# Performance work log

Measured on AMD Instinct MI355X. Metric: run time of the kernel, lower is better.

Reference implementation:

```python
import jax, jax.numpy as jnp
import numpy as np

B, T, N, E = 32, 512, 4, 16          # batch, seq_len, num_nodes, num_edges (N*N)
NI, EI = 16, 8                        # node / edge input channels
HN, HE, MH, C = 128, 128, 256, 8      # hidden node/edge, mlp hidden, classes

# complete-graph edge list (matches the src/dst double loop in __init__)
SRC = np.repeat(np.arange(N), N)      # [E]
DST = np.tile(np.arange(N), N)        # [E]
# GCNConv (PyG default) adds self-loops on top of the existing complete graph
# -> adjacency counts: off-diag 1, diag 2; in-degree of every node = N+1.
# symmetric norm deg^-1/2 A deg^-1/2 collapses to A/(N+1). Dense 4x4 matmul
# per graph is the efficient faithful form of the scatter-add here.
NORM_ADJ = (np.ones((N, N), np.float32) + np.eye(N, dtype=np.float32)) / (N + 1)


def lstm(x, Wih, Whh, b):
    """batch_first LSTM, torch gate order (i,f,g,o). x: [Bn,T,D] -> [Bn,T,H]."""
    H = Whh.shape[0]
    xz = x @ Wih + b  # precompute input projection [Bn,T,4H]

    def step(carry, zt):
        h, c = carry
        z = zt + h @ Whh
        i, f, g, o = jnp.split(z, 4, axis=-1)
        c = jax.nn.sigmoid(f) * c + jax.nn.sigmoid(i) * jnp.tanh(g)
        h = jax.nn.sigmoid(o) * jnp.tanh(c)
        return (h, c), h

    init = (jnp.zeros((x.shape[0], H), x.dtype), jnp.zeros((x.shape[0], H), x.dtype))
    _, hs = jax.lax.scan(step, init, jnp.swapaxes(xz, 0, 1))
    return jnp.swapaxes(hs, 0, 1)


def setup_inputs() -> dict:
    key = jax.random.key(0)
    ks = jax.random.split(key, 30)

    def p(k, shape, s=0.05):
        return (jax.random.normal(k, shape, jnp.float32) * s)

    return {
        "x_seq": jax.random.normal(ks[0], (B, T, N, NI), jnp.float32),
        "edge_attr_seq": jax.random.normal(ks[1], (B, T, E, EI), jnp.float32),
        "Wn1": p(ks[2], (NI, HN)), "bn1": p(ks[3], (HN,)),
        "Wn2": p(ks[4], (HN, HN)), "bn2": p(ks[5], (HN,)),
        "We1": p(ks[6], (EI, HE)), "be1": p(ks[7], (HE,)),
        "We2": p(ks[8], (HE, HE)), "be2": p(ks[9], (HE,)),
        "Wg1": p(ks[10], (HN, HN)), "bg1": p(ks[11], (HN,)),
        "Wg2": p(ks[12], (HN, HN)), "bg2": p(ks[13], (HN,)),
        "Wef1": p(ks[14], (HE, HE)), "bef1": p(ks[15], (HE,)),
        "Wef2": p(ks[16], (HE, HE)), "bef2": p(ks[17], (HE,)),
        "Wih_n": p(ks[18], (HN, 4 * HN)), "Whh_n": p(ks[19], (HN, 4 * HN)), "b_n": p(ks[20], (4 * HN,)),
        "Wih_e": p(ks[21], (HE, 4 * HE)), "Whh_e": p(ks[22], (HE, 4 * HE)), "b_e": p(ks[23], (4 * HE,)),
        "Wc1": p(ks[24], (2 * HN + HE, MH)), "bc1": p(ks[25], (MH,)),
        "Wc2": p(ks[26], (MH, C)), "bc2": p(ks[27], (C,)),
    }


def reference(x_seq, edge_attr_seq, Wn1, bn1, Wn2, bn2, We1, be1, We2, be2,
              Wg1, bg1, Wg2, bg2, Wef1, bef1, Wef2, bef2,
              Wih_n, Whh_n, b_n, Wih_e, Whh_e, b_e, Wc1, bc1, Wc2, bc2):
    adj = jnp.asarray(NORM_ADJ)
    # node / edge MLP embeddings
    x = jax.nn.relu(jax.nn.relu(x_seq @ Wn1 + bn1) @ Wn2 + bn2)      # [B,T,N,HN]
    e = jax.nn.relu(jax.nn.relu(edge_attr_seq @ We1 + be1) @ We2 + be2)  # [B,T,E,HE]
    # two GCN layers: normalized-adjacency aggregation per (batch,time) graph
    x = jax.nn.relu(jnp.einsum('ij,btjd->btid', adj, x @ Wg1) + bg1)
    x = jax.nn.relu(jnp.einsum('ij,btjd->btid', adj, x @ Wg2) + bg2)
    # edge FC stack
    e = jax.nn.relu(jax.nn.relu(e @ Wef1 + bef1) @ Wef2 + bef2)
    # LSTMs over time, one sequence per (batch, node) / (batch, edge)
    xn = x.transpose(0, 2, 1, 3).reshape(B * N, T, HN)
    en = e.transpose(0, 2, 1, 3).reshape(B * E, T, HE)
    hn = lstm(xn, Wih_n, Whh_n, b_n).reshape(B, N, T, HN).transpose(0, 2, 1, 3)  # [B,T,N,HN]
    he = lstm(en, Wih_e, Whh_e, b_e).reshape(B, E, T, HE).transpose(0, 2, 1, 3)  # [B,T,E,HE]
    # edge-gather classifier
    src_f = hn[:, :, jnp.asarray(SRC), :]
    dst_f = hn[:, :, jnp.asarray(DST), :]
    feats = jnp.concatenate([src_f, dst_f, he], axis=-1)  # [B,T,E,2HN+HE]
    logits = jax.nn.relu(feats @ Wc1 + bc1) @ Wc2 + bc2   # [B,T,E,C]
    return logits
```

## Files before the change

kernel.cpp:

```cpp
#include <hip/hip_runtime.h>
#include <cstdint>

constexpr int T_  = 512;
constexpr int HN_ = 128;

#define DEVI __device__ __forceinline__

typedef __bf16 bf16x8 __attribute__((ext_vector_type(8)));
typedef __bf16 bf16x4 __attribute__((ext_vector_type(4)));
typedef float  f32x4  __attribute__((ext_vector_type(4)));

DEVI float sigf(float x) { return __builtin_amdgcn_rcpf(1.f + __expf(-x)); }
DEVI float tanh_fast(float x) {
  return 1.f - 2.f * __builtin_amdgcn_rcpf(1.f + __expf(2.f * x));
}

DEVI void layer128_bf(const __bf16* __restrict__ src, __bf16* __restrict__ dst,
                      bf16x8 w0, bf16x8 w1, bf16x8 w2, bf16x8 w3,
                      float bv, int lm, int lh, int n)
{
  #pragma unroll
  for (int m = 0; m < 4; ++m) {
    const __bf16* sp = &src[(m*16 + lm)*136 + lh*8];
    const bf16x8 a0 = *reinterpret_cast<const bf16x8*>(sp);
    const bf16x8 a1 = *reinterpret_cast<const bf16x8*>(sp + 32);
    const bf16x8 a2 = *reinterpret_cast<const bf16x8*>(sp + 64);
    const bf16x8 a3 = *reinterpret_cast<const bf16x8*>(sp + 96);
    f32x4 acc = { bv, bv, bv, bv };
    acc = __builtin_amdgcn_mfma_f32_16x16x32_bf16(a0, w0, acc, 0, 0, 0);
    acc = __builtin_amdgcn_mfma_f32_16x16x32_bf16(a1, w1, acc, 0, 0, 0);
    acc = __builtin_amdgcn_mfma_f32_16x16x32_bf16(a2, w2, acc, 0, 0, 0);
    acc = __builtin_amdgcn_mfma_f32_16x16x32_bf16(a3, w3, acc, 0, 0, 0);
    #pragma unroll
    for (int r = 0; r < 4; ++r)
      dst[(m*16 + lh*4 + r)*136 + n] = (__bf16)fmaxf(acc[r], 0.f);
  }
}

DEVI void layer128_f32(const __bf16* __restrict__ src, float* __restrict__ dst,
                       bf16x8 w0, bf16x8 w1, bf16x8 w2, bf16x8 w3,
                       float bv, bool relu, int lm, int lh, int n)
{
  #pragma unroll
  for (int m = 0; m < 4; ++m) {
    const __bf16* sp = &src[(m*16 + lm)*136 + lh*8];
    const bf16x8 a0 = *reinterpret_cast<const bf16x8*>(sp);
    const bf16x8 a1 = *reinterpret_cast<const bf16x8*>(sp + 32);
    const bf16x8 a2 = *reinterpret_cast<const bf16x8*>(sp + 64);
    const bf16x8 a3 = *reinterpret_cast<const bf16x8*>(sp + 96);
    f32x4 acc = { bv, bv, bv, bv };
    acc = __builtin_amdgcn_mfma_f32_16x16x32_bf16(a0, w0, acc, 0, 0, 0);
    acc = __builtin_amdgcn_mfma_f32_16x16x32_bf16(a1, w1, acc, 0, 0, 0);
    acc = __builtin_amdgcn_mfma_f32_16x16x32_bf16(a2, w2, acc, 0, 0, 0);
    acc = __builtin_amdgcn_mfma_f32_16x16x32_bf16(a3, w3, acc, 0, 0, 0);
    #pragma unroll
    for (int r = 0; r < 4; ++r)
      dst[(m*16 + lh*4 + r)*132 + n] = relu ? fmaxf(acc[r], 0.f) : acc[r];
  }
}

__global__ __launch_bounds__(512, 4) void node_mlp_mfma_kernel(
    const float* __restrict__ x_seq,
    const float* __restrict__ Wn1, const float* __restrict__ bn1,
    const float* __restrict__ Wn2, const float* __restrict__ bn2,
    const float* __restrict__ Wg1, const float* __restrict__ bg1,
    const float* __restrict__ Wg2, const float* __restrict__ bg2,
    __bf16* __restrict__ xn)
{
  constexpr int P1 = 40;
  __shared__ __align__(16) __bf16 A1[64 * P1];
  __shared__ __align__(16) __bf16 Ab[64 * 136];
  __shared__ __align__(16) __bf16 Bb[64 * 136];
  __shared__ __align__(16) float  Yf[64 * 132];

  const int tid = threadIdx.x;
  const int w = tid >> 6, l = tid & 63, lm = l & 15, lh = l >> 4;
  const int n = w*16 + lm;

  bf16x8 w1, w2[4], w3[4], w4[4];
  const float b1 = bn1[n], b2 = bn2[n];
  #pragma unroll
  for (int j = 0; j < 8; ++j) {
    const int k = lh*8 + j;
    w1[j] = (k < 16) ? (__bf16)Wn1[k*128 + n] : (__bf16)0.f;
  }
  #pragma unroll
  for (int kt = 0; kt < 4; ++kt)
    #pragma unroll
    for (int j = 0; j < 8; ++j) {
      const int k = kt*32 + lh*8 + j;
      w2[kt][j] = (__bf16)Wn2[k*128 + n];
      w3[kt][j] = (__bf16)Wg1[k*128 + n];
      w4[kt][j] = (__bf16)Wg2[k*128 + n];
    }

  for (int i = tid; i < 64 * P1; i += 512) A1[i] = (__bf16)0.f;

  for (int g = blockIdx.x; g < 1024; g += 512) {
    #pragma unroll
    for (int it = 0; it < 2; ++it) {
      const int i = tid + it*512;
      A1[(i >> 4)*P1 + (i & 15)] = (__bf16)x_seq[(size_t)g*1024 + i];
    }
    __syncthreads();
    #pragma unroll
    for (int m = 0; m < 4; ++m) {
      const bf16x8 a = *reinterpret_cast<const bf16x8*>(&A1[(m*16+lm)*P1 + lh*8]);
      f32x4 acc = { b1, b1, b1, b1 };
      acc = __builtin_amdgcn_mfma_f32_16x16x32_bf16(a, w1, acc, 0, 0, 0);
      #pragma unroll
      for (int r = 0; r < 4; ++r)
        Ab[(m*16 + lh*4 + r)*136 + n] = (__bf16)fmaxf(acc[r], 0.f);
    }
    __syncthreads();
    layer128_bf(Ab, Bb, w2[0], w2[1], w2[2], w2[3], b2, lm, lh, n);
    __syncthreads();
    layer128_f32(Bb, Yf, w3[0], w3[1], w3[2], w3[3], 0.f, false, lm, lh, n);
    __syncthreads();
    #pragma unroll
    for (int it = 0; it < 4; ++it) {
      const int idx = tid + it*512;
      const int q = idx >> 7, d = idx & 127;
      const float y0 = Yf[(q*4+0)*132 + d], y1 = Yf[(q*4+1)*132 + d];
      const float y2 = Yf[(q*4+2)*132 + d], y3 = Yf[(q*4+3)*132 + d];
      const float s = y0 + y1 + y2 + y3;
      const float bv = bg1[d];
      Ab[(q*4+0)*136 + d] = (__bf16)fmaxf((s + y0)*0.2f + bv, 0.f);
      Ab[(q*4+1)*136 + d] = (__bf16)fmaxf((s + y1)*0.2f + bv, 0.f);
      Ab[(q*4+2)*136 + d] = (__bf16)fmaxf((s + y2)*0.2f + bv, 0.f);
      Ab[(q*4+3)*136 + d] = (__bf16)fmaxf((s + y3)*0.2f + bv, 0.f);
    }
    __syncthreads();
    layer128_f32(Ab, Yf, w4[0], w4[1], w4[2], w4[3], 0.f, false, lm, lh, n);
    __syncthreads();
    #pragma unroll
    for (int it = 0; it < 4; ++it) {
      const int idx = tid + it*512;
      const int q = idx >> 7, d = idx & 127;
      const int bt = g*16 + q, bb = bt >> 9, tt = bt & 511;
      const float y0 = Yf[(q*4+0)*132 + d], y1 = Yf[(q*4+1)*132 + d];
      const float y2 = Yf[(q*4+2)*132 + d], y3 = Yf[(q*4+3)*132 + d];
      const float s = y0 + y1 + y2 + y3;
      const float bv = bg2[d];
      xn[((size_t)(bb*4+0)*T_ + tt)*HN_ + d] = (__bf16)fmaxf((s + y0)*0.2f + bv, 0.f);
      xn[((size_t)(bb*4+1)*T_ + tt)*HN_ + d] = (__bf16)fmaxf((s + y1)*0.2f + bv, 0.f);
      xn[((size_t)(bb*4+2)*T_ + tt)*HN_ + d] = (__bf16)fmaxf((s + y2)*0.2f + bv, 0.f);
      xn[((size_t)(bb*4+3)*T_ + tt)*HN_ + d] = (__bf16)fmaxf((s + y3)*0.2f + bv, 0.f);
    }
    __syncthreads();
  }
}

__global__ __launch_bounds__(512, 4) void edge_mlp_mfma_kernel(
    const float* __restrict__ ea,
    const float* __restrict__ We1, const float* __restrict__ be1,
    const float* __restrict__ We2, const float* __restrict__ be2,
    const float* __restrict__ Wef1, const float* __restrict__ bef1,
    const float* __restrict__ Wef2, const float* __restrict__ bef2,
    __bf16* __restrict__ en)
{
  constexpr int P1 = 40;
  __shared__ __align__(16) __bf16 A1[64 * P1];
  __shared__ __align__(16) __bf16 Ab[64 * 136];
  __shared__ __align__(16) __bf16 Bb[64 * 136];
  __shared__ __align__(16) float  Of[64 * 132];

  const int tid = threadIdx.x;
  const int w = tid >> 6, l = tid & 63, lm = l & 15, lh = l >> 4;
  const int n = w*16 + lm;

  bf16x8 w1, w2[4], w3[4], w4[4];
  const float b1 = be1[n], b2 = be2[n], b3 = bef1[n], b4 = bef2[n];
  #pragma unroll
  for (int j = 0; j < 8; ++j) {
    const int k = lh*8 + j;
    w1[j] = (k < 8) ? (__bf16)We1[k*128 + n] : (__bf16)0.f;
  }
  #pragma unroll
  for (int kt = 0; kt < 4; ++kt)
    #pragma unroll
    for (int j = 0; j < 8; ++j) {
      const int k = kt*32 + lh*8 + j;
      w2[kt][j] = (__bf16)We2[k*128 + n];
      w3[kt][j] = (__bf16)Wef1[k*128 + n];
      w4[kt][j] = (__bf16)Wef2[k*128 + n];
    }

  for (int i = tid; i < 64 * P1; i += 512) A1[i] = (__bf16)0.f;

  for (int g = blockIdx.x; g < 4096; g += 512) {
    A1[(tid >> 3)*P1 + (tid & 7)] = (__bf16)ea[(size_t)g*512 + tid];
    __syncthreads();
    #pragma unroll
    for (int m = 0; m < 4; ++m) {
      const bf16x8 a = *reinterpret_cast<const bf16x8*>(&A1[(m*16+lm)*P1 + lh*8]);
      f32x4 acc = { b1, b1, b1, b1 };
      acc = __builtin_amdgcn_mfma_f32_16x16x32_bf16(a, w1, acc, 0, 0, 0);
      #pragma unroll
      for (int r = 0; r < 4; ++r)
        Ab[(m*16 + lh*4 + r)*136 + n] = (__bf16)fmaxf(acc[r], 0.f);
    }
    __syncthreads();
    layer128_bf(Ab, Bb, w2[0], w2[1], w2[2], w2[3], b2, lm, lh, n);
    __syncthreads();
    layer128_bf(Bb, Ab, w3[0], w3[1], w3[2], w3[3], b3, lm, lh, n);
    __syncthreads();
    layer128_f32(Ab, Of, w4[0], w4[1], w4[2], w4[3], b4, true, lm, lh, n);
    __syncthreads();
    #pragma unroll
    for (int i = 0; i < 4; ++i) {
      const int fi = tid + i*512;
      const int row = fi >> 5, c4 = fi & 31;
      const int q = row >> 4, e = row & 15;
      const int bt = g*4 + q, bb = bt >> 9, tt = bt & 511;
      const float4 v = *reinterpret_cast<const float4*>(&Of[row*132 + c4*4]);
      bf16x4 pk;
      pk[0]=(__bf16)v.x; pk[1]=(__bf16)v.y; pk[2]=(__bf16)v.z; pk[3]=(__bf16)v.w;
      *reinterpret_cast<bf16x4*>(
          &en[((size_t)(bb*16+e)*T_ + tt)*HN_ + c4*4]) = pk;
    }
    __syncthreads();
  }
}

__global__ __launch_bounds__(512, 2) void lstm_mfma_kernel(
    const float* __restrict__ Wih_n, const float* __restrict__ Whh_n,
    const float* __restrict__ b_n,
    const float* __restrict__ Wih_e, const float* __restrict__ Whh_e,
    const float* __restrict__ b_e,
    __bf16* __restrict__ xn, __bf16* __restrict__ en)
{
  __shared__ __align__(16) __bf16 ring[16 * 16 * 128];

  const bool is_node = (int)blockIdx.x < 8;
  const int  bidx    = is_node ? blockIdx.x : ((int)blockIdx.x - 8);
  const float* __restrict__ Wih  = is_node ? Wih_n : Wih_e;
  const float* __restrict__ Whh  = is_node ? Whh_n : Whh_e;
  const float* __restrict__ bias = is_node ? b_n   : b_e;
  __bf16* __restrict__ xh = (is_node ? xn : en) + (size_t)bidx * 16 * (T_ * HN_);

  const int tid = threadIdx.x;
  const int w   = tid >> 6;
  const int l   = tid & 63;
  const int lm  = l & 15;
  const int lh  = l >> 4;

  bf16x8 wih_f[4][4], whh_f[4][4];
  f32x4  bias_v[4];
  #pragma unroll
  for (int nt = 0; nt < 4; ++nt) {
    const int d   = w*16 + nt*4 + lh;
    bias_v[nt][0] = bias[0*128 + d];
    bias_v[nt][1] = bias[1*128 + d];
    bias_v[nt][2] = bias[2*128 + d];
    bias_v[nt][3] = bias[3*128 + d];
    const int col = (lm & 3)*128 + w*16 + nt*4 + (lm >> 2);
    #pragma unroll
    for (int kt = 0; kt < 4; ++kt)
      #pragma unroll
      for (int j = 0; j < 8; ++j) {
        const int k = kt*32 + lh*8 + j;
        wih_f[nt][kt][j] = (__bf16)Wih[k*512 + col];
        whh_f[nt][kt][j] = (__bf16)Whh[k*512 + col];
      }
  }

  {
    bf16x4 z; z[0]=z[1]=z[2]=z[3]=(__bf16)0.f;
    *reinterpret_cast<bf16x4*>(&ring[15*2048 + tid*4]) = z;
  }
  __syncthreads();

  const size_t seqStride = (size_t)T_ * HN_;
  const __bf16* __restrict__ xseq = xh + (size_t)lm * seqStride;

  f32x4 accsX[4];
  {
    bf16x8 bx[4];
    #pragma unroll
    for (int kt = 0; kt < 4; ++kt)
      bx[kt] = *reinterpret_cast<const bf16x8*>(&xseq[kt*32 + lh*8]);
    #pragma unroll
    for (int nt = 0; nt < 4; ++nt) {
      accsX[nt] = bias_v[nt];
      #pragma unroll
      for (int kt = 0; kt < 4; ++kt)
        accsX[nt] = __builtin_amdgcn_mfma_f32_16x16x32_bf16(wih_f[nt][kt], bx[kt], accsX[nt], 0, 0, 0);
    }
  }
  bf16x8 bxO[4], bxE[4];
  #pragma unroll
  for (int kt = 0; kt < 4; ++kt)
    bxO[kt] = *reinterpret_cast<const bf16x8*>(&xseq[(size_t)1*HN_ + kt*32 + lh*8]);

  float c[4] = {0.f, 0.f, 0.f, 0.f};

  #pragma unroll 2
  for (int t = 0; t < T_; ++t) {
    bf16x8* bxLoad = (t & 1) ? bxO : bxE;
    bf16x8* bxUse  = (t & 1) ? bxE : bxO;
    {
      const int tp = (t + 2 < T_) ? t + 2 : T_ - 1;
      #pragma unroll
      for (int kt = 0; kt < 4; ++kt)
        bxLoad[kt] = *reinterpret_cast<const bf16x8*>(
            &xseq[(size_t)tp*HN_ + kt*32 + lh*8]);
    }

    const int rbase = ((t + 15) & 15)*2048 + lm*128;
    bf16x8 bh[4];
    #pragma unroll
    for (int kt = 0; kt < 4; ++kt)
      bh[kt] = *reinterpret_cast<const bf16x8*>(
          &ring[rbase + (((kt*4 + lh) ^ (lm & 7)) << 3)]);

    #pragma unroll
    for (int nt = 0; nt < 4; ++nt)
      #pragma unroll
      for (int kt = 0; kt < 4; ++kt)
        accsX[nt] = __builtin_amdgcn_mfma_f32_16x16x32_bf16(whh_f[nt][kt], bh[kt], accsX[nt], 0, 0, 0);

    const int wbase = (t & 15)*2048 + lm*128;
    #pragma unroll
    for (int nt = 0; nt < 4; ++nt) {
      const float zi = accsX[nt][0], zf = accsX[nt][1];
      const float zg = accsX[nt][2], zo = accsX[nt][3];
      c[nt] = sigf(zf)*c[nt] + sigf(zi)*tanh_fast(zg);
      const float h = sigf(zo)*tanh_fast(c[nt]);
      const int up = (2*w + (nt >> 1)) ^ (lm & 7);
      ring[wbase + up*8 + (nt & 1)*4 + lh] = (__bf16)h;
    }

    #pragma unroll
    for (int nt = 0; nt < 4; ++nt) {
      accsX[nt] = bias_v[nt];
      #pragma unroll
      for (int kt = 0; kt < 4; ++kt)
        accsX[nt] = __builtin_amdgcn_mfma_f32_16x16x32_bf16(wih_f[nt][kt], bxUse[kt], accsX[nt], 0, 0, 0);
    }
    __syncthreads();

    if ((t & 15) == 15) {
      const int tb = t - 15;
      #pragma unroll
      for (int i = 0; i < 8; ++i) {
        const int uf = tid + i*512;
        const int tl = uf >> 8, sq = (uf >> 4) & 15, us = uf & 15;
        const int ulog = us ^ (sq & 7);
        const bf16x8 v = *reinterpret_cast<const bf16x8*>(
            &ring[tl*2048 + sq*128 + us*8]);
        *reinterpret_cast<bf16x8*>(
            &xh[(size_t)sq*seqStride + (size_t)(tb + tl)*HN_ + ulog*8]) = v;
      }
      __syncthreads();
    }
  }
}

__global__ __launch_bounds__(512, 1) void classifier_mfma_kernel(
    const __bf16* __restrict__ hn, const __bf16* __restrict__ he,
    const float* __restrict__ Wc1, const float* __restrict__ bc1,
    const float* __restrict__ Wc2, const float* __restrict__ bc2,
    float* __restrict__ out)
{
  constexpr int HP = 136;
  constexpr int DP = 264;
  __shared__ __align__(16) __bf16 hn_l[32 * HP];
  __shared__ __align__(16) __bf16 he_l[128 * HP];
  __shared__ __align__(16) __bf16 hid_l[128 * DP];

  const int tid = threadIdx.x;
  const int w   = tid >> 6;
  const int l   = tid & 63;
  const int lm  = l & 15;
  const int lh  = l >> 4;

  bf16x8 wb[2][12];
  float  bcol[2];
  #pragma unroll
  for (int jt = 0; jt < 2; ++jt) {
    const int j = w*32 + jt*16 + lm;
    bcol[jt] = bc1[j];
    #pragma unroll
    for (int kt = 0; kt < 12; ++kt)
      #pragma unroll
      for (int i = 0; i < 8; ++i)
        wb[jt][kt][i] = (__bf16)Wc1[(kt*32 + lh*8 + i)*256 + j];
  }
  bf16x8 wc2f[8];
  const float bc2v = (lm < 8) ? bc2[lm] : 0.f;
  #pragma unroll
  for (int kt = 0; kt < 8; ++kt)
    #pragma unroll
    for (int i = 0; i < 8; ++i)
      wc2f[kt][i] = (lm < 8) ? (__bf16)Wc2[(kt*32 + lh*8 + i)*8 + lm] : (__bf16)0.f;

  for (int g = blockIdx.x; g < 2048; g += 256) {
    const int b  = g >> 6;
    const int t0 = (g & 63) * 8;

    for (int u = tid; u < 2048; u += 512) {
      const int e = u >> 7, rem = u & 127;
      const int tt = rem >> 4, k = (rem & 15)*8;
      const bf16x8 v = *reinterpret_cast<const bf16x8*>(
          &he[((size_t)(b*16+e)*T_ + t0 + tt)*HN_ + k]);
      *reinterpret_cast<bf16x8*>(&he_l[(tt*16 + e)*HP + k]) = v;
    }
    for (int u = tid; u < 512; u += 512) {
      const int n = u >> 7, rem = u & 127;
      const int tt = rem >> 4, k = (rem & 15)*8;
      const bf16x8 v = *reinterpret_cast<const bf16x8*>(
          &hn[((size_t)(b*4+n)*T_ + t0 + tt)*HN_ + k]);
      *reinterpret_cast<bf16x8*>(&hn_l[(tt*4 + n)*HP + k]) = v;
    }
    __syncthreads();

    for (int tt = 0; tt < 8; ++tt) {
      bf16x8 af[12];
      #pragma unroll
      for (int kt = 0; kt < 4; ++kt)
        af[kt] = *reinterpret_cast<const bf16x8*>(
            &hn_l[(tt*4 + (lm>>2))*HP + kt*32 + lh*8]);
      #pragma unroll
      for (int kt = 0; kt < 4; ++kt)
        af[4+kt] = *reinterpret_cast<const bf16x8*>(
            &hn_l[(tt*4 + (lm&3))*HP + kt*32 + lh*8]);
      #pragma unroll
      for (int kt = 0; kt < 4; ++kt)
        af[8+kt] = *reinterpret_cast<const bf16x8*>(
            &he_l[(tt*16 + lm)*HP + kt*32 + lh*8]);
      #pragma unroll
      for (int jt = 0; jt < 2; ++jt) {
        f32x4 acc = { bcol[jt], bcol[jt], bcol[jt], bcol[jt] };
        #pragma unroll
        for (int kt = 0; kt < 12; ++kt)
          acc = __builtin_amdgcn_mfma_f32_16x16x32_bf16(af[kt], wb[jt][kt], acc, 0, 0, 0);
        #pragma unroll
        for (int r = 0; r < 4; ++r)
          hid_l[(tt*16 + lh*4 + r)*DP + (w*2 + jt)*16 + lm] = (__bf16)fmaxf(acc[r], 0.f);
      }
    }
    __syncthreads();

    {
      const int tt = w;
      f32x4 acc = { bc2v, bc2v, bc2v, bc2v };
      #pragma unroll
      for (int kt = 0; kt < 8; ++kt) {
        const bf16x8 a = *reinterpret_cast<const bf16x8*>(
            &hid_l[(tt*16 + lm)*DP + kt*32 + lh*8]);
        acc = __builtin_amdgcn_mfma_f32_16x16x32_bf16(a, wc2f[kt], acc, 0, 0, 0);
      }
      if (lm < 8) {
        const size_t bt = (size_t)b*T_ + t0 + tt;
        #pragma unroll
        for (int r = 0; r < 4; ++r)
          out[(bt*16 + lh*4 + r)*8 + lm] = acc[r];
      }
    }
    __syncthreads();
  }
}

extern "C" void kernel_launch(void* const* d_in, const int* in_sizes, int n_in,
                              void* d_out, int out_size, void* d_ws, size_t ws_size,
                              hipStream_t stream) {
  (void)in_sizes; (void)n_in; (void)out_size; (void)ws_size;
  const float* x_seq = (const float*)d_in[0];
  const float* ea    = (const float*)d_in[1];
  const float* Wn1 = (const float*)d_in[2];
  const float* bn1 = (const float*)d_in[3];
  const float* Wn2 = (const float*)d_in[4];
  const float* bn2 = (const float*)d_in[5];
  const float* We1 = (const float*)d_in[6];
  const float* be1 = (const float*)d_in[7];
  const float* We2 = (const float*)d_in[8];
  const float* be2 = (const float*)d_in[9];
  const float* Wg1 = (const float*)d_in[10];
  const float* bg1 = (const float*)d_in[11];
  const float* Wg2 = (const float*)d_in[12];
  const float* bg2 = (const float*)d_in[13];
  const float* Wef1 = (const float*)d_in[14];
  const float* bef1 = (const float*)d_in[15];
  const float* Wef2 = (const float*)d_in[16];
  const float* bef2 = (const float*)d_in[17];
  const float* Wih_n = (const float*)d_in[18];
  const float* Whh_n = (const float*)d_in[19];
  const float* b_n   = (const float*)d_in[20];
  const float* Wih_e = (const float*)d_in[21];
  const float* Whh_e = (const float*)d_in[22];
  const float* b_e   = (const float*)d_in[23];
  const float* Wc1 = (const float*)d_in[24];
  const float* bc1 = (const float*)d_in[25];
  const float* Wc2 = (const float*)d_in[26];
  const float* bc2 = (const float*)d_in[27];

  __bf16* xn = (__bf16*)d_ws;
  __bf16* en = xn + (size_t)128 * T_ * HN_;
  float* out = (float*)d_out;

  node_mlp_mfma_kernel<<<512, 512, 0, stream>>>(x_seq, Wn1, bn1, Wn2, bn2,
                                                Wg1, bg1, Wg2, bg2, xn);
  edge_mlp_mfma_kernel<<<512, 512, 0, stream>>>(ea, We1, be1, We2, be2,
                                                Wef1, bef1, Wef2, bef2, en);
  lstm_mfma_kernel<<<40, 512, 0, stream>>>(Wih_n, Whh_n, b_n,
                                           Wih_e, Whh_e, b_e, xn, en);
  classifier_mfma_kernel<<<256, 512, 0, stream>>>(xn, en, Wc1, bc1, Wc2, bc2, out);
}
```

Measured before the change: 779.5 us.

## Stage LSTM input chunks into LDS via async global_load_lds per 16 steps

The LSTM kernel now loads each 16-timestep chunk of input activations for all 16 sequences into a new LDS buffer with global_load_lds, instead of each lane issuing per-step global loads with a two-step register prefetch. The time loop is restructured into 16-step chunks with a fully unrolled inner loop, and the input projection for step t+1 is computed before the gate nonlinearities of step t. Writeback of hidden states is folded into the chunk boundary. Doubling LDS use drops occupancy to one block per CU, and each chunk adds a load-then-barrier stall that is not overlapped with compute.

```diff
diff --git a/kernel.cpp b/kernel.cpp
--- a/kernel.cpp
+++ b/kernel.cpp
@@ -223,14 +223,15 @@
   }
 }
 
-__global__ __launch_bounds__(512, 2) void lstm_mfma_kernel(
+__global__ __launch_bounds__(512, 1) void lstm_mfma_kernel(
     const float* __restrict__ Wih_n, const float* __restrict__ Whh_n,
     const float* __restrict__ b_n,
     const float* __restrict__ Wih_e, const float* __restrict__ Whh_e,
     const float* __restrict__ b_e,
     __bf16* __restrict__ xn, __bf16* __restrict__ en)
 {
-  __shared__ __align__(16) __bf16 ring[16 * 16 * 128];
+  __shared__ __align__(16) __bf16 x_c[16 * 2048];
+  __shared__ __align__(16) __bf16 ring[16 * 2048];
 
   const bool is_node = (int)blockIdx.x < 8;
   const int  bidx    = is_node ? blockIdx.x : ((int)blockIdx.x - 8);
@@ -269,79 +270,18 @@
     bf16x4 z; z[0]=z[1]=z[2]=z[3]=(__bf16)0.f;
     *reinterpret_cast<bf16x4*>(&ring[15*2048 + tid*4]) = z;
   }
-  __syncthreads();
 
   const size_t seqStride = (size_t)T_ * HN_;
-  const __bf16* __restrict__ xseq = xh + (size_t)lm * seqStride;
-
+  int fsw[4];
+  #pragma unroll
+  for (int kt = 0; kt < 4; ++kt) fsw[kt] = (((kt*4 + lh) ^ (lm & 7)) << 3);
+
+  float c[4] = {0.f, 0.f, 0.f, 0.f};
   f32x4 accsX[4];
-  {
-    bf16x8 bx[4];
-    #pragma unroll
-    for (int kt = 0; kt < 4; ++kt)
-      bx[kt] = *reinterpret_cast<const bf16x8*>(&xseq[kt*32 + lh*8]);
-    #pragma unroll
-    for (int nt = 0; nt < 4; ++nt) {
-      accsX[nt] = bias_v[nt];
-      #pragma unroll
-      for (int kt = 0; kt < 4; ++kt)
-        accsX[nt] = __builtin_amdgcn_mfma_f32_16x16x32_bf16(wih_f[nt][kt], bx[kt], accsX[nt], 0, 0, 0);
-    }
-  }
-  bf16x8 bxO[4], bxE[4];
-  #pragma unroll
-  for (int kt = 0; kt < 4; ++kt)
-    bxO[kt] = *reinterpret_cast<const bf16x8*>(&xseq[(size_t)1*HN_ + kt*32 + lh*8]);
-
-  float c[4] = {0.f, 0.f, 0.f, 0.f};
-
-  #pragma unroll 2
-  for (int t = 0; t < T_; ++t) {
-    bf16x8* bxLoad = (t & 1) ? bxO : bxE;
-    bf16x8* bxUse  = (t & 1) ? bxE : bxO;
-    {
-      const int tp = (t + 2 < T_) ? t + 2 : T_ - 1;
-      #pragma unroll
-      for (int kt = 0; kt < 4; ++kt)
-        bxLoad[kt] = *reinterpret_cast<const bf16x8*>(
-            &xseq[(size_t)tp*HN_ + kt*32 + lh*8]);
-    }
-
-    const int rbase = ((t + 15) & 15)*2048 + lm*128;
-    bf16x8 bh[4];
-    #pragma unroll
-    for (int kt = 0; kt < 4; ++kt)
-      bh[kt] = *reinterpret_cast<const bf16x8*>(
-          &ring[rbase + (((kt*4 + lh) ^ (lm & 7)) << 3)]);
-
-    #pragma unroll
-    for (int nt = 0; nt < 4; ++nt)
-      #pragma unroll
-      for (int kt = 0; kt < 4; ++kt)
-        accsX[nt] = __builtin_amdgcn_mfma_f32_16x16x32_bf16(whh_f[nt][kt], bh[kt], accsX[nt], 0, 0, 0);
-
-    const int wbase = (t & 15)*2048 + lm*128;
-    #pragma unroll
-    for (int nt = 0; nt < 4; ++nt) {
-      const float zi = accsX[nt][0], zf = accsX[nt][1];
-      const float zg = accsX[nt][2], zo = accsX[nt][3];
-      c[nt] = sigf(zf)*c[nt] + sigf(zi)*tanh_fast(zg);
-      const float h = sigf(zo)*tanh_fast(c[nt]);
-      const int up = (2*w + (nt >> 1)) ^ (lm & 7);
-      ring[wbase + up*8 + (nt & 1)*4 + lh] = (__bf16)h;
-    }
-
-    #pragma unroll
-    for (int nt = 0; nt < 4; ++nt) {
-      accsX[nt] = bias_v[nt];
-      #pragma unroll
-      for (int kt = 0; kt < 4; ++kt)
-        accsX[nt] = __builtin_amdgcn_mfma_f32_16x16x32_bf16(wih_f[nt][kt], bxUse[kt], accsX[nt], 0, 0, 0);
-    }
-    __syncthreads();
-
-    if ((t & 15) == 15) {
-      const int tb = t - 15;
+
+  #pragma unroll 1
+  for (int t0 = 0; t0 < T_; t0 += 16) {
+    if (t0) {
       #pragma unroll
       for (int i = 0; i < 8; ++i) {
         const int uf = tid + i*512;
@@ -350,10 +290,94 @@
         const bf16x8 v = *reinterpret_cast<const bf16x8*>(
             &ring[tl*2048 + sq*128 + us*8]);
         *reinterpret_cast<bf16x8*>(
-            &xh[(size_t)sq*seqStride + (size_t)(tb + tl)*HN_ + ulog*8]) = v;
+            &xh[(size_t)sq*seqStride + (size_t)(t0-16+tl)*HN_ + ulog*8]) = v;
+      }
+    }
+    #pragma unroll
+    for (int it = 0; it < 8; ++it) {
+      const int U   = tid + it*512;
+      const int seq = U >> 8, rem = U & 255;
+      const int tl2 = rem >> 4, v = rem & 15;
+      const __bf16* src = &xh[(size_t)seq*seqStride + (size_t)(t0+tl2)*HN_
+                              + ((v ^ (seq & 7)) << 3)];
+      const int Ubase = (tid & ~63) + it*512;
+      __builtin_amdgcn_global_load_lds(
+          (const __attribute__((address_space(1))) void*)src,
+          (__attribute__((address_space(3))) void*)&x_c[Ubase*8], 16, 0, 0);
+    }
+    __syncthreads();
+
+    {
+      bf16x8 bx[4];
+      #pragma unroll
+      for (int kt = 0; kt < 4; ++kt)
+        bx[kt] = *reinterpret_cast<const bf16x8*>(&x_c[lm*2048 + fsw[kt]]);
+      #pragma unroll
+      for (int nt = 0; nt < 4; ++nt) {
+        accsX[nt] = bias_v[nt];
+        #pragma unroll
+        for (int kt = 0; kt < 4; ++kt)
+          accsX[nt] = __builtin_amdgcn_mfma_f32_16x16x32_bf16(wih_f[nt][kt], bx[kt], accsX[nt], 0, 0, 0);
+      }
+    }
+
+    #pragma unroll
+    for (int tl = 0; tl < 16; ++tl) {
+      const int rbase = ((tl + 15) & 15)*2048 + lm*128;
+      bf16x8 bh[4];
+      #pragma unroll
+      for (int kt = 0; kt < 4; ++kt)
+        bh[kt] = *reinterpret_cast<const bf16x8*>(&ring[rbase + fsw[kt]]);
+
+      #pragma unroll
+      for (int nt = 0; nt < 4; ++nt)
+        #pragma unroll
+        for (int kt = 0; kt < 4; ++kt)
+          accsX[nt] = __builtin_amdgcn_mfma_f32_16x16x32_bf16(whh_f[nt][kt], bh[kt], accsX[nt], 0, 0, 0);
+
+      f32x4 accN[4];
+      if (tl < 15) {
+        bf16x8 bx[4];
+        #pragma unroll
+        for (int kt = 0; kt < 4; ++kt)
+          bx[kt] = *reinterpret_cast<const bf16x8*>(
+              &x_c[lm*2048 + (tl+1)*128 + fsw[kt]]);
+        #pragma unroll
+        for (int nt = 0; nt < 4; ++nt) {
+          accN[nt] = bias_v[nt];
+          #pragma unroll
+          for (int kt = 0; kt < 4; ++kt)
+            accN[nt] = __builtin_amdgcn_mfma_f32_16x16x32_bf16(wih_f[nt][kt], bx[kt], accN[nt], 0, 0, 0);
+        }
+      }
+
+      const int wbase = tl*2048 + lm*128;
+      #pragma unroll
+      for (int nt = 0; nt < 4; ++nt) {
+        const float zi = accsX[nt][0], zf = accsX[nt][1];
+        const float zg = accsX[nt][2], zo = accsX[nt][3];
+        c[nt] = sigf(zf)*c[nt] + sigf(zi)*tanh_fast(zg);
+        const float h = sigf(zo)*tanh_fast(c[nt]);
+        const int up = (2*w + (nt >> 1)) ^ (lm & 7);
+        ring[wbase + up*8 + (nt & 1)*4 + lh] = (__bf16)h;
+      }
+
+      if (tl < 15) {
+        #pragma unroll
+        for (int nt = 0; nt < 4; ++nt) accsX[nt] = accN[nt];
       }
       __syncthreads();
     }
+  }
+  #pragma unroll
+  for (int i = 0; i < 8; ++i) {
+    const int uf = tid + i*512;
+    const int tl = uf >> 8, sq = (uf >> 4) & 15, us = uf & 15;
+    const int ulog = us ^ (sq & 7);
+    const bf16x8 v = *reinterpret_cast<const bf16x8*>(
+        &ring[tl*2048 + sq*128 + us*8]);
+    *reinterpret_cast<bf16x8*>(
+        &xh[(size_t)sq*seqStride + (size_t)(T_-16+tl)*HN_ + ulog*8]) = v;
   }
 }
 
```

Measured after the change: 774.3 us. About the same (-0.7%).
